# Kernel optimization log

Hardware: AMD Instinct MI355X
Metric: run time of the kernel (lower is better)

## Reference

```python
import jax, jax.numpy as jnp
import numpy as np

DIM = 64
K = 7
GC = 8            # groups_channels (hardcoded in module)
G = DIM // GC     # groups = 8
RED = 2           # reduction_ratio
PAD = (K - 1) // 2


def _patches(y, k, p):
    # torch nn.Unfold(k, dilation=1, padding=p, stride=1) ordering: (c, kh, kw)
    b, c, H, W = y.shape
    yp = jnp.pad(y, ((0, 0), (0, 0), (p, p), (p, p)))
    tiles = [yp[:, :, i:i + H, j:j + W] for i in range(k) for j in range(k)]
    return jnp.stack(tiles, axis=2)  # (b, c, k*k, H, W)


def setup_inputs() -> dict:
    key = jax.random.key(0)
    ks = jax.random.split(key, 6)
    b, h, w = 4, 128, 128
    input_x = jax.random.normal(ks[0], (b, DIM, h, w), dtype=jnp.float32)
    input_y = jax.random.normal(ks[1], (b, DIM, h, w), dtype=jnp.float32)
    c_mid = DIM // RED
    w1 = jax.random.normal(ks[2], (c_mid, DIM), dtype=jnp.float32) * 0.05
    b1 = jnp.zeros((c_mid,), dtype=jnp.float32)
    w2 = jax.random.normal(ks[3], (K * K * G, c_mid), dtype=jnp.float32) * 0.05
    b2 = jnp.zeros((K * K * G,), dtype=jnp.float32)
    return {"input_x": input_x, "input_y": input_y, "w1": w1, "b1": b1, "w2": w2, "b2": b2}


def reference(input_x, input_y, w1, b1, w2, b2):
    b, c, h, w = input_x.shape
    # 1x1 convs generating dynamic kernels (stride == 1, no avgpool)
    mid = jnp.einsum('bchw,oc->bohw', input_x, w1) + b1[None, :, None, None]
    weight = jnp.einsum('bchw,oc->bohw', mid, w2) + b2[None, :, None, None]
    # (b, G, 1, k*k, h, w) broadcast over groups_channels
    weight = weight.reshape(b, G, K * K, h, w)[:, :, None]
    # unfold input_y -> (b, G, GC, k*k, h, w)
    out = _patches(input_y, K, PAD).reshape(b, G, GC, K * K, h, w)
    out = (weight * out).sum(axis=3).reshape(b, DIM, h, w)
    return out
```

## Files before the change

### kernel.cpp

```cpp
#include <hip/hip_runtime.h>
#include <hip/hip_fp16.h>

#define DIMC 64
#define KS 7
#define NTAP 49
#define GCH 8
#define NG 8
#define CMID 32
#define PADD 3
#define HH 128
#define WW 128
#define PLANE (HH*WW)
#define TW 32
#define TH 8
#define TPX (TW+2*PADD)
#define TPY (TH+2*PADD)
#define NPIX (TPX*TPY)
#define NB 4
#define WTSTR 54
#define CPAD 12

#define WC_OFF 0
#define BC_OFF 65536
#define XT_OFF 67584
#define WS_NEED (XT_OFF + (size_t)NB * PLANE * DIMC * 2)

typedef __attribute__((ext_vector_type(8))) short short8;
typedef __attribute__((ext_vector_type(4))) float f32x4;
typedef __fp16 fp16x2 __attribute__((ext_vector_type(2)));

static __device__ inline unsigned short f2bs(float f) {
    union { float f; unsigned u; } v; v.f = f;
    unsigned r = v.u + 0x7fff + ((v.u >> 16) & 1);
    return (unsigned short)(r >> 16);
}

static __device__ inline unsigned pkh(float a, float b) {
    union { fp16x2 h; unsigned u; } c;
    c.h = __builtin_amdgcn_cvt_pkrtz(a, b);
    return c.u;
}

__global__ __launch_bounds__(256)
void prep_all(const float* __restrict__ x,
              const float* __restrict__ w1, const float* __restrict__ b1,
              const float* __restrict__ w2, const float* __restrict__ b2,
              unsigned short* __restrict__ wc, float* __restrict__ bc,
              unsigned short* __restrict__ xt) {
    const int bid = blockIdx.x;
    if (bid < 512) {
        const int pxblk = bid & 63, rest = bid >> 6;
        const int b = rest & 3, h = rest >> 2;
        const int px = pxblk * 256 + threadIdx.x;
        const float* xp = x + (size_t)b * DIMC * PLANE + (size_t)h * 32 * PLANE + px;
        #pragma unroll
        for (int q = 0; q < 4; ++q) {
            unsigned pk[4];
            #pragma unroll
            for (int j = 0; j < 4; ++j) {
                float v0 = xp[(size_t)(q * 8 + 2 * j) * PLANE];
                float v1 = xp[(size_t)(q * 8 + 2 * j + 1) * PLANE];
                pk[j] = ((unsigned)f2bs(v1) << 16) | f2bs(v0);
            }
            *reinterpret_cast<uint4*>(xt + (((size_t)b * 8 + h * 4 + q) * PLANE + px) * 8) =
                make_uint4(pk[0], pk[1], pk[2], pk[3]);
        }
    } else {
        const int idx = (bid - 512) * 256 + threadIdx.x;
        const int row64 = idx >> 4;
        const int c0 = (idx & 15) * 4;
        const int g = row64 >> 6, r = row64 & 63;
        float a0 = 0.f, a1 = 0.f, a2 = 0.f, a3 = 0.f, bv = 0.f;
        if (r < NTAP) {
            const float* w2r = w2 + (g * NTAP + r) * CMID;
            #pragma unroll
            for (int m = 0; m < CMID; ++m) {
                float wv = w2r[m];
                const float* w1r = w1 + m * DIMC + c0;
                a0 = fmaf(wv, w1r[0], a0);
                a1 = fmaf(wv, w1r[1], a1);
                a2 = fmaf(wv, w1r[2], a2);
                a3 = fmaf(wv, w1r[3], a3);
            }
            if (c0 == 0) {
                bv = b2[g * NTAP + r];
                #pragma unroll
                for (int m = 0; m < CMID; ++m) bv = fmaf(w2r[m], b1[m], bv);
            }
        }
        *reinterpret_cast<uint2*>(wc + row64 * DIMC + c0) =
            make_uint2(((unsigned)f2bs(a1) << 16) | f2bs(a0),
                       ((unsigned)f2bs(a3) << 16) | f2bs(a2));
        if ((idx & 15) == 0) bc[row64] = bv;
    }
}

__global__ __launch_bounds__(256, 4)
void invol_mfma3_kernel(const float* __restrict__ y,
                        const unsigned short* __restrict__ xt,
                        const unsigned short* __restrict__ wc,
                        const float* __restrict__ bc,
                        float* __restrict__ out) {
    __shared__ __half ytile[NPIX * GCH];
    __shared__ __half wtl[256 * WTSTR];

    const int tid = threadIdx.x;
    const int l = tid & 63, w = tid >> 6;
    const int bx = blockIdx.x, by = blockIdx.y;
    const int b = blockIdx.z >> 3, g = blockIdx.z & 7;

    #pragma unroll
    for (int k = 0; k < 5; ++k) {
        int i = tid + k * 256;
        if (i < NPIX * 2) {
            int q  = i / NPIX;
            int px = i - q * NPIX;
            int c0 = q * 4;
            int r = px / TPX, col = px - r * TPX;
            int sy = by * TH + r - PADD, sx = bx * TW + col - PADD;
            bool ok = (sy >= 0 && sy < HH && sx >= 0 && sx < WW);
            const float* yp = y + ((size_t)(b * DIMC + g * GCH + c0) * HH + sy) * WW + sx;
            float v0 = ok ? yp[0] : 0.f;
            float v1 = ok ? yp[PLANE] : 0.f;
            float v2 = ok ? yp[2 * PLANE] : 0.f;
            float v3 = ok ? yp[3 * PLANE] : 0.f;
            *reinterpret_cast<uint2*>(&ytile[px * GCH + c0]) =
                make_uint2(pkh(v0, v1), pkh(v2, v3));
        }
    }

    const int fr = l & 15, fk = l >> 4;
    f32x4 acc[4][4];
    #pragma unroll
    for (int mt = 0; mt < 4; ++mt)
        #pragma unroll
        for (int nt = 0; nt < 4; ++nt)
            acc[mt][nt] = f32x4{0.f, 0.f, 0.f, 0.f};

    int gpix[4];
    #pragma unroll
    for (int nt = 0; nt < 4; ++nt) {
        int lp = w * 64 + nt * 16 + fr;
        gpix[nt] = (by * TH + (lp >> 5)) * WW + bx * TW + (lp & 31);
    }

    #pragma unroll
    for (int kp = 0; kp < 2; ++kp) {
        short8 af[4];
        #pragma unroll
        for (int mt = 0; mt < 4; ++mt) {
            union { uint4 u; short8 s; } cv;
            cv.u = *reinterpret_cast<const uint4*>(
                wc + ((size_t)(g * 64 + mt * 16 + fr)) * DIMC + kp * 32 + fk * 8);
            af[mt] = cv.s;
        }
        short8 bf[4];
        #pragma unroll
        for (int nt = 0; nt < 4; ++nt) {
            union { uint4 u; short8 s; } cv;
            cv.u = *reinterpret_cast<const uint4*>(
                xt + (((size_t)b * 8 + kp * 4 + fk) * PLANE + gpix[nt]) * 8);
            bf[nt] = cv.s;
        }
        #pragma unroll
        for (int mt = 0; mt < 4; ++mt)
            #pragma unroll
            for (int nt = 0; nt < 4; ++nt)
                acc[mt][nt] = __builtin_amdgcn_mfma_f32_16x16x32_bf16(
                    af[mt], bf[nt], acc[mt][nt], 0, 0, 0);
    }

    const int r0 = fk * 4;
    #pragma unroll
    for (int mt = 0; mt < 4; ++mt) {
        if (mt < 3 || r0 == 0) {
            int rb = mt * 16 + r0;
            float bb0 = bc[g * 64 + rb + 0], bb1 = bc[g * 64 + rb + 1];
            float bb2 = bc[g * 64 + rb + 2], bb3 = bc[g * 64 + rb + 3];
            #pragma unroll
            for (int nt = 0; nt < 4; ++nt) {
                int lp = w * 64 + nt * 16 + fr;
                *reinterpret_cast<uint2*>(&wtl[lp * WTSTR + rb]) =
                    make_uint2(pkh(acc[mt][nt][0] + bb0, acc[mt][nt][1] + bb1),
                               pkh(acc[mt][nt][2] + bb2, acc[mt][nt][3] + bb3));
            }
        }
    }

    __syncthreads();

    __half2 wth[26];
    const __half2* wrow = reinterpret_cast<const __half2*>(&wtl[tid * WTSTR]);
    #pragma unroll
    for (int q = 0; q < 26; ++q) wth[q] = wrow[q];

    const int tx = tid & 31, ty = tid >> 5;
    __half2 acch[4];
    #pragma unroll
    for (int cc = 0; cc < 4; ++cc) acch[cc] = __float2half2_rn(0.f);
    #pragma unroll
    for (int ky = 0; ky < KS; ++ky) {
        #pragma unroll
        for (int kx = 0; kx < KS; ++kx) {
            const int kk = ky * KS + kx;
            __half wh = (kk & 1) ? __high2half(wth[kk >> 1]) : __low2half(wth[kk >> 1]);
            __half2 wv2 = __half2half2(wh);
            int pp = (ty + ky) * TPX + (tx + kx);
            union { uint4 u; __half2 h[4]; } yv;
            yv.u = *reinterpret_cast<const uint4*>(&ytile[pp * GCH]);
            acch[0] = __hfma2(wv2, yv.h[0], acch[0]);
            acch[1] = __hfma2(wv2, yv.h[1], acch[1]);
            acch[2] = __hfma2(wv2, yv.h[2], acch[2]);
            acch[3] = __hfma2(wv2, yv.h[3], acch[3]);
        }
    }

    const int gy = by * TH + ty, gx = bx * TW + tx;
    float* op = out + ((size_t)(b * DIMC + g * GCH) * HH + gy) * WW + gx;
    #pragma unroll
    for (int cc = 0; cc < 4; ++cc) {
        float2 f = __half22float2(acch[cc]);
        op[(2 * cc) * PLANE]     = f.x;
        op[(2 * cc + 1) * PLANE] = f.y;
    }
}

__global__ __launch_bounds__(256, 1)
void invol_fused_kernel(const float* __restrict__ x, const float* __restrict__ y,
                        const float* __restrict__ w1, const float* __restrict__ b1,
                        const float* __restrict__ w2, const float* __restrict__ b2,
                        float* __restrict__ out) {
    __shared__ float ytile[NPIX * CPAD];
    const int tid = threadIdx.x;
    const int tx = tid & 31, ty = tid >> 5;
    const int bx = blockIdx.x, by = blockIdx.y, bz = blockIdx.z;
    const int gx = bx * TW + tx, gy = by * TH + ty;

    float xv[DIMC];
    const float* xp = x + ((size_t)(bz * DIMC) * HH + gy) * WW + gx;
    #pragma unroll
    for (int c = 0; c < DIMC; ++c) xv[c] = xp[c * PLANE];

    float mid[CMID];
    #pragma unroll
    for (int m = 0; m < CMID; ++m) {
        float a = b1[m];
        const float4* w1r = reinterpret_cast<const float4*>(w1 + m * DIMC);
        #pragma unroll
        for (int cq = 0; cq < DIMC / 4; ++cq) {
            float4 wv = w1r[cq];
            a = fmaf(wv.x, xv[4*cq+0], a);
            a = fmaf(wv.y, xv[4*cq+1], a);
            a = fmaf(wv.z, xv[4*cq+2], a);
            a = fmaf(wv.w, xv[4*cq+3], a);
        }
        mid[m] = a;
    }

    for (int g = 0; g < NG; ++g) {
        __syncthreads();
        for (int i = tid; i < NPIX * GCH; i += 256) {
            int c = i / NPIX;
            int p = i - c * NPIX;
            int r = p / TPX;
            int col = p - r * TPX;
            int sy = by * TH + r - PADD;
            int sx = bx * TW + col - PADD;
            float v = 0.f;
            if (sy >= 0 && sy < HH && sx >= 0 && sx < WW)
                v = y[((size_t)(bz * DIMC + g * GCH + c) * HH + sy) * WW + sx];
            ytile[p * CPAD + c] = v;
        }
        __syncthreads();

        float wt[NTAP];
        const float*  b2g = b2 + g * NTAP;
        const float4* w2g = reinterpret_cast<const float4*>(w2 + g * NTAP * CMID);
        #pragma unroll
        for (int kk = 0; kk < NTAP; ++kk) {
            float a = b2g[kk];
            #pragma unroll
            for (int mq = 0; mq < CMID / 4; ++mq) {
                float4 wv = w2g[kk * (CMID / 4) + mq];
                a = fmaf(wv.x, mid[4*mq+0], a);
                a = fmaf(wv.y, mid[4*mq+1], a);
                a = fmaf(wv.z, mid[4*mq+2], a);
                a = fmaf(wv.w, mid[4*mq+3], a);
            }
            wt[kk] = a;
        }

        float acc[GCH];
        #pragma unroll
        for (int cc = 0; cc < GCH; ++cc) acc[cc] = 0.f;
        #pragma unroll
        for (int ky = 0; ky < KS; ++ky) {
            #pragma unroll
            for (int kx = 0; kx < KS; ++kx) {
                float wv = wt[ky * KS + kx];
                int pp = (ty + ky) * TPX + (tx + kx);
                const float4* yr = reinterpret_cast<const float4*>(&ytile[pp * CPAD]);
                float4 ya = yr[0];
                float4 yb = yr[1];
                acc[0] = fmaf(wv, ya.x, acc[0]);
                acc[1] = fmaf(wv, ya.y, acc[1]);
                acc[2] = fmaf(wv, ya.z, acc[2]);
                acc[3] = fmaf(wv, ya.w, acc[3]);
                acc[4] = fmaf(wv, yb.x, acc[4]);
                acc[5] = fmaf(wv, yb.y, acc[5]);
                acc[6] = fmaf(wv, yb.z, acc[6]);
                acc[7] = fmaf(wv, yb.w, acc[7]);
            }
        }

        float* op = out + ((size_t)(bz * DIMC + g * GCH) * HH + gy) * WW + gx;
        #pragma unroll
        for (int cc = 0; cc < GCH; ++cc) op[cc * PLANE] = acc[cc];
    }
}

extern "C" void kernel_launch(void* const* d_in, const int* in_sizes, int n_in,
                              void* d_out, int out_size, void* d_ws, size_t ws_size,
                              hipStream_t stream) {
    const float* x  = (const float*)d_in[0];
    const float* y  = (const float*)d_in[1];
    const float* w1 = (const float*)d_in[2];
    const float* b1 = (const float*)d_in[3];
    const float* w2 = (const float*)d_in[4];
    const float* b2 = (const float*)d_in[5];
    float* out = (float*)d_out;

    if (ws_size >= WS_NEED) {
        char* ws = (char*)d_ws;
        unsigned short* wcp = (unsigned short*)(ws + WC_OFF);
        float*          bcp = (float*)(ws + BC_OFF);
        unsigned short* xtp = (unsigned short*)(ws + XT_OFF);

        hipLaunchKernelGGL(prep_all, dim3(512 + 32), dim3(256), 0, stream,
                           x, w1, b1, w2, b2, wcp, bcp, xtp);
        hipLaunchKernelGGL(invol_mfma3_kernel, dim3(WW / TW, HH / TH, NB * NG), dim3(256), 0, stream,
                           y, xtp, wcp, bcp, out);
    } else {
        dim3 grid(WW / TW, HH / TH, NB);
        hipLaunchKernelGGL(invol_fused_kernel, grid, dim3(256), 0, stream,
                           x, y, w1, b1, w2, b2, out);
    }
}
```

Before: 38.96 us.

## Split dynamic-weight MFMA into two halves to shrink LDS and raise occupancy

The 64 dynamic weight rows are now generated in two chunks of 32, each staged through a smaller LDS buffer (stride 36 instead of 54) and consumed by the 7x7 involution before the next chunk. The global loads of the y tile and of the B fragments are issued up front and held in registers so their latency overlaps other work. Launch bounds rise to 5 blocks per CU. In exchange the kernel adds extra __syncthreads per chunk and keeps more values live in registers.

```diff
diff --git a/kernel.cpp b/kernel.cpp
--- a/kernel.cpp
+++ b/kernel.cpp
@@ -17,7 +17,7 @@
 #define TPY (TH+2*PADD)
 #define NPIX (TPX*TPY)
 #define NB 4
-#define WTSTR 54
+#define WTSTR 36
 #define CPAD 12
 
 #define WC_OFF 0
@@ -95,8 +95,8 @@
     }
 }
 
-__global__ __launch_bounds__(256, 4)
-void invol_mfma3_kernel(const float* __restrict__ y,
+__global__ __launch_bounds__(256, 5)
+void invol_mfma4_kernel(const float* __restrict__ y,
                         const unsigned short* __restrict__ xt,
                         const unsigned short* __restrict__ wc,
                         const float* __restrict__ bc,
@@ -106,36 +106,27 @@
 
     const int tid = threadIdx.x;
     const int l = tid & 63, w = tid >> 6;
+    const int fr = l & 15, fk = l >> 4;
     const int bx = blockIdx.x, by = blockIdx.y;
     const int b = blockIdx.z >> 3, g = blockIdx.z & 7;
-
+    const int tx = tid & 31, ty = tid >> 5;
+
+    float yv[5][4];
+    int   yoff[5];
     #pragma unroll
     for (int k = 0; k < 5; ++k) {
         int i = tid + k * 256;
-        if (i < NPIX * 2) {
-            int q  = i / NPIX;
-            int px = i - q * NPIX;
-            int c0 = q * 4;
-            int r = px / TPX, col = px - r * TPX;
-            int sy = by * TH + r - PADD, sx = bx * TW + col - PADD;
-            bool ok = (sy >= 0 && sy < HH && sx >= 0 && sx < WW);
-            const float* yp = y + ((size_t)(b * DIMC + g * GCH + c0) * HH + sy) * WW + sx;
-            float v0 = ok ? yp[0] : 0.f;
-            float v1 = ok ? yp[PLANE] : 0.f;
-            float v2 = ok ? yp[2 * PLANE] : 0.f;
-            float v3 = ok ? yp[3 * PLANE] : 0.f;
-            *reinterpret_cast<uint2*>(&ytile[px * GCH + c0]) =
-                make_uint2(pkh(v0, v1), pkh(v2, v3));
-        }
-    }
-
-    const int fr = l & 15, fk = l >> 4;
-    f32x4 acc[4][4];
-    #pragma unroll
-    for (int mt = 0; mt < 4; ++mt)
-        #pragma unroll
-        for (int nt = 0; nt < 4; ++nt)
-            acc[mt][nt] = f32x4{0.f, 0.f, 0.f, 0.f};
+        bool act = (i < NPIX * 2);
+        int q  = i / NPIX;
+        int px = i - q * NPIX;
+        int r = px / TPX, col = px - r * TPX;
+        int sy = by * TH + r - PADD, sx = bx * TW + col - PADD;
+        bool ok = act && sy >= 0 && sy < HH && sx >= 0 && sx < WW;
+        const float* yp = y + ((size_t)(b * DIMC + g * GCH + q * 4) * HH + sy) * WW + sx;
+        #pragma unroll
+        for (int j = 0; j < 4; ++j) yv[k][j] = ok ? yp[j * PLANE] : 0.f;
+        yoff[k] = act ? (px * GCH + q * 4) : -1;
+    }
 
     int gpix[4];
     #pragma unroll
@@ -143,75 +134,96 @@
         int lp = w * 64 + nt * 16 + fr;
         gpix[nt] = (by * TH + (lp >> 5)) * WW + bx * TW + (lp & 31);
     }
-
-    #pragma unroll
-    for (int kp = 0; kp < 2; ++kp) {
-        short8 af[4];
-        #pragma unroll
-        for (int mt = 0; mt < 4; ++mt) {
-            union { uint4 u; short8 s; } cv;
-            cv.u = *reinterpret_cast<const uint4*>(
-                wc + ((size_t)(g * 64 + mt * 16 + fr)) * DIMC + kp * 32 + fk * 8);
-            af[mt] = cv.s;
-        }
-        short8 bf[4];
+    short8 bf[2][4];
+    #pragma unroll
+    for (int kp = 0; kp < 2; ++kp)
         #pragma unroll
         for (int nt = 0; nt < 4; ++nt) {
             union { uint4 u; short8 s; } cv;
             cv.u = *reinterpret_cast<const uint4*>(
                 xt + (((size_t)b * 8 + kp * 4 + fk) * PLANE + gpix[nt]) * 8);
-            bf[nt] = cv.s;
-        }
-        #pragma unroll
-        for (int mt = 0; mt < 4; ++mt)
+            bf[kp][nt] = cv.s;
+        }
+
+    #pragma unroll
+    for (int k = 0; k < 5; ++k) {
+        if (yoff[k] >= 0) {
+            *reinterpret_cast<uint2*>(&ytile[yoff[k]]) =
+                make_uint2(pkh(yv[k][0], yv[k][1]), pkh(yv[k][2], yv[k][3]));
+        }
+    }
+
+    __half2 acch[4];
+    #pragma unroll
+    for (int cc = 0; cc < 4; ++cc) acch[cc] = __float2half2_rn(0.f);
+    const int ybase = (ty * TPX + tx) * GCH;
+
+    #pragma unroll
+    for (int mc = 0; mc < 2; ++mc) {
+        f32x4 acc[2][4];
+        #pragma unroll
+        for (int dm = 0; dm < 2; ++dm)
             #pragma unroll
             for (int nt = 0; nt < 4; ++nt)
-                acc[mt][nt] = __builtin_amdgcn_mfma_f32_16x16x32_bf16(
-                    af[mt], bf[nt], acc[mt][nt], 0, 0, 0);
-    }
-
-    const int r0 = fk * 4;
-    #pragma unroll
-    for (int mt = 0; mt < 4; ++mt) {
-        if (mt < 3 || r0 == 0) {
-            int rb = mt * 16 + r0;
+                acc[dm][nt] = f32x4{0.f, 0.f, 0.f, 0.f};
+
+        #pragma unroll
+        for (int dm = 0; dm < 2; ++dm) {
+            short8 af[2];
+            #pragma unroll
+            for (int kp = 0; kp < 2; ++kp) {
+                union { uint4 u; short8 s; } cv;
+                cv.u = *reinterpret_cast<const uint4*>(
+                    wc + ((size_t)(g * 64 + (mc * 2 + dm) * 16 + fr)) * DIMC + kp * 32 + fk * 8);
+                af[kp] = cv.s;
+            }
+            #pragma unroll
+            for (int kp = 0; kp < 2; ++kp)
+                #pragma unroll
+                for (int nt = 0; nt < 4; ++nt)
+                    acc[dm][nt] = __builtin_amdgcn_mfma_f32_16x16x32_bf16(
+                        af[kp], bf[kp][nt], acc[dm][nt], 0, 0, 0);
+        }
+
+        __syncthreads();
+
+        #pragma unroll
+        for (int dm = 0; dm < 2; ++dm) {
+            int rb = (mc * 2 + dm) * 16 + fk * 4;
             float bb0 = bc[g * 64 + rb + 0], bb1 = bc[g * 64 + rb + 1];
             float bb2 = bc[g * 64 + rb + 2], bb3 = bc[g * 64 + rb + 3];
             #pragma unroll
             for (int nt = 0; nt < 4; ++nt) {
                 int lp = w * 64 + nt * 16 + fr;
-                *reinterpret_cast<uint2*>(&wtl[lp * WTSTR + rb]) =
-                    make_uint2(pkh(acc[mt][nt][0] + bb0, acc[mt][nt][1] + bb1),
-                               pkh(acc[mt][nt][2] + bb2, acc[mt][nt][3] + bb3));
-            }
-        }
-    }
-
-    __syncthreads();
-
-    __half2 wth[26];
-    const __half2* wrow = reinterpret_cast<const __half2*>(&wtl[tid * WTSTR]);
-    #pragma unroll
-    for (int q = 0; q < 26; ++q) wth[q] = wrow[q];
-
-    const int tx = tid & 31, ty = tid >> 5;
-    __half2 acch[4];
-    #pragma unroll
-    for (int cc = 0; cc < 4; ++cc) acch[cc] = __float2half2_rn(0.f);
-    #pragma unroll
-    for (int ky = 0; ky < KS; ++ky) {
-        #pragma unroll
-        for (int kx = 0; kx < KS; ++kx) {
-            const int kk = ky * KS + kx;
-            __half wh = (kk & 1) ? __high2half(wth[kk >> 1]) : __low2half(wth[kk >> 1]);
+                *reinterpret_cast<uint2*>(&wtl[lp * WTSTR + dm * 16 + fk * 4]) =
+                    make_uint2(pkh(acc[dm][nt][0] + bb0, acc[dm][nt][1] + bb1),
+                               pkh(acc[dm][nt][2] + bb2, acc[dm][nt][3] + bb3));
+            }
+        }
+
+        __syncthreads();
+
+        uint2 wr[8];
+        #pragma unroll
+        for (int q = 0; q < 8; ++q)
+            wr[q] = *reinterpret_cast<const uint2*>(&wtl[tid * WTSTR + q * 4]);
+
+        const int ninv = (mc == 0) ? 32 : 17;
+        #pragma unroll
+        for (int j = 0; j < 32; ++j) {
+            if (j >= ninv) break;
+            const int kk = mc * 32 + j;
+            const int ky = kk / 7, kx = kk - ky * 7;
+            unsigned uh = (j & 2) ? wr[j >> 2].y : wr[j >> 2].x;
+            union { unsigned u; __half2 h; } hc; hc.u = uh;
+            __half wh = (j & 1) ? __high2half(hc.h) : __low2half(hc.h);
             __half2 wv2 = __half2half2(wh);
-            int pp = (ty + ky) * TPX + (tx + kx);
-            union { uint4 u; __half2 h[4]; } yv;
-            yv.u = *reinterpret_cast<const uint4*>(&ytile[pp * GCH]);
-            acch[0] = __hfma2(wv2, yv.h[0], acch[0]);
-            acch[1] = __hfma2(wv2, yv.h[1], acch[1]);
-            acch[2] = __hfma2(wv2, yv.h[2], acch[2]);
-            acch[3] = __hfma2(wv2, yv.h[3], acch[3]);
+            union { uint4 u; __half2 h[4]; } yvv;
+            yvv.u = *reinterpret_cast<const uint4*>(&ytile[ybase + (ky * TPX + kx) * GCH]);
+            acch[0] = __hfma2(wv2, yvv.h[0], acch[0]);
+            acch[1] = __hfma2(wv2, yvv.h[1], acch[1]);
+            acch[2] = __hfma2(wv2, yvv.h[2], acch[2]);
+            acch[3] = __hfma2(wv2, yvv.h[3], acch[3]);
         }
     }
 
@@ -338,7 +350,7 @@
 
         hipLaunchKernelGGL(prep_all, dim3(512 + 32), dim3(256), 0, stream,
                            x, w1, b1, w2, b2, wcp, bcp, xtp);
-        hipLaunchKernelGGL(invol_mfma3_kernel, dim3(WW / TW, HH / TH, NB * NG), dim3(256), 0, stream,
+        hipLaunchKernelGGL(invol_mfma4_kernel, dim3(WW / TW, HH / TH, NB * NG), dim3(256), 0, stream,
                            y, xtp, wcp, bcp, out);
     } else {
         dim3 grid(WW / TW, HH / TH, NB);
```

Result: faster. 34.47 us (-11.5%).
